# Kernel optimization log

Hardware: AMD Instinct MI355X
Metric: run time of the kernel (lower is better)

## Reference

```python
import jax, jax.numpy as jnp
import numpy as np

KQ_SIZE = 256  # kq_size from init


def setup_inputs() -> dict:
    key = jax.random.key(0)
    ks = jax.random.split(key, 8)
    B, N, V, KQ = 8, 4096, 1024, KQ_SIZE
    return {
        "input": jax.random.normal(ks[0], (B, N, V), dtype=jnp.float32),
        "Wq": jax.random.normal(ks[1], (V, KQ), dtype=jnp.float32) * 0.02,
        "bq": jax.random.normal(ks[2], (V,), dtype=jnp.float32) * 0.02,
        "Wk": jax.random.normal(ks[3], (V, KQ), dtype=jnp.float32) * 0.02,
        "bk": jax.random.normal(ks[4], (V,), dtype=jnp.float32) * 0.02,
        "Wv": jax.random.normal(ks[5], (V, V), dtype=jnp.float32) * 0.02,
        "bv": jax.random.normal(ks[6], (V,), dtype=jnp.float32) * 0.02,
        "gamma": jax.random.normal(ks[7], (1,), dtype=jnp.float32),
    }


def reference(input, Wq, bq, Wk, bk, Wv, bv, gamma):
    # input: [B, N, V]; flag=False -> kq slice is the LAST KQ_SIZE features
    kq = input[:, :, -KQ_SIZE:]                      # [B, N, KQ]
    q = jnp.einsum('bnk,vk->bnv', kq, Wq) + bq        # [B, N, V]
    k = jnp.einsum('bnk,vk->bnv', kq, Wk) + bk        # [B, N, V]
    v = jnp.einsum('bne,ve->bnv', input, Wv) + bv     # [B, N, V]
    # attn = bmm(k^T, q): feature-feature attention, NO 1/sqrt(d) scale
    attn = jnp.einsum('bnv,bnw->bvw', k, q)           # [B, V, V]
    attn = jax.nn.softmax(attn, axis=-1)
    out = jnp.einsum('bnv,bvw->bnw', v, attn)         # [B, N, V]
    return gamma * out + input
```

## Files before the change

### kernel.cpp

```cpp
#include <hip/hip_runtime.h>

#define B_ 8
#define N_ 4096
#define V_ 1024
#define KQ_ 256
#define KQOFF 768

typedef unsigned short u16;
typedef unsigned int u32;
typedef __attribute__((ext_vector_type(8))) __bf16 bf16x8;
typedef __attribute__((ext_vector_type(4))) float f32x4;

__device__ __forceinline__ u16 f2bf(float f) {
    union { float f; u32 u; } v; v.f = f;
    u32 r = v.u + 0x7fffu + ((v.u >> 16) & 1u);
    return (u16)(r >> 16);
}
__device__ __forceinline__ float bf2f(u16 h) {
    union { u32 u; float f; } v; v.u = ((u32)h) << 16; return v.f;
}
__device__ __forceinline__ void gl_lds16(const void* g, void* l) {
    __builtin_amdgcn_global_load_lds((const __attribute__((address_space(1))) u32*)g,
                                     (__attribute__((address_space(3))) u32*)l, 16, 0, 0);
}


__global__ void k_sum_s(const float* __restrict__ in, float* __restrict__ s) {
    const int b = blockIdx.x, chunk = blockIdx.y, k = threadIdx.x;
    const float* p = in + ((size_t)b * N_ + (size_t)chunk * 256) * V_ + KQOFF + k;
    float acc = 0.f;
    for (int r = 0; r < 256; ++r) acc += p[(size_t)r * V_];
    atomicAdd(&s[b * KQ_ + k], acc);
}

__global__ void k_syrk(const float* __restrict__ in, float* __restrict__ S) {
    const int bz = blockIdx.z;
    const int b = bz >> 3, nc = bz & 7;
    const int i0 = blockIdx.x * 64, j0 = blockIdx.y * 64;
    __shared__ float As[16][64], Bs[16][64];
    const int tid = threadIdx.x, tx = tid & 15, ty = tid >> 4;
    const int lrow = tid >> 4, lcol = (tid & 15) * 4;
    float acc[4][4] = {};
    const float* Xb = in + (size_t)b * N_ * V_ + KQOFF;
    const int nbeg = nc * 512, nend = nbeg + 512;
    for (int n0 = nbeg; n0 < nend; n0 += 16) {
        const float* base = Xb + (size_t)(n0 + lrow) * V_;
        const float4 a4 = *(const float4*)(base + i0 + lcol);
        const float4 b4 = *(const float4*)(base + j0 + lcol);
        *(float4*)&As[lrow][lcol] = a4;
        *(float4*)&Bs[lrow][lcol] = b4;
        __syncthreads();
#pragma unroll
        for (int kk = 0; kk < 16; ++kk) {
            float ra[4], rb[4];
#pragma unroll
            for (int a = 0; a < 4; ++a) ra[a] = As[kk][ty * 4 + a];
#pragma unroll
            for (int q = 0; q < 4; ++q) rb[q] = Bs[kk][tx * 4 + q];
#pragma unroll
            for (int a = 0; a < 4; ++a)
#pragma unroll
                for (int q = 0; q < 4; ++q) acc[a][q] += ra[a] * rb[q];
        }
        __syncthreads();
    }
#pragma unroll
    for (int a = 0; a < 4; ++a)
#pragma unroll
        for (int q = 0; q < 4; ++q)
            atomicAdd(&S[((size_t)b * KQ_ + i0 + ty * 4 + a) * KQ_ + j0 + tx * 4 + q],
                      acc[a][q]);
}

__global__ void k_uv(const float* __restrict__ Wq, const float* __restrict__ Wk,
                     const float* __restrict__ s, float* __restrict__ u,
                     float* __restrict__ t) {
    const int b = blockIdx.x;
    const int w = blockIdx.y * 256 + threadIdx.x;
    __shared__ float sl[256];
    sl[threadIdx.x] = s[b * KQ_ + threadIdx.x];
    __syncthreads();
    float au = 0.f, at = 0.f;
    const float* qr = Wq + (size_t)w * KQ_;
    const float* kr = Wk + (size_t)w * KQ_;
    for (int i = 0; i < KQ_; ++i) { au += qr[i] * sl[i]; at += kr[i] * sl[i]; }
    u[b * V_ + w] = au;
    t[b * V_ + w] = at;
}

__global__ void k_wkS(const float* __restrict__ Wk, const float* __restrict__ S,
                      float* __restrict__ T) {
    const int b = blockIdx.z;
    const int i0 = blockIdx.x * 64, j0 = blockIdx.y * 64;
    __shared__ float As[64][17];
    __shared__ float Bs[16][64];
    const int tid = threadIdx.x, tx = tid & 15, ty = tid >> 4;
    const int ar = tid >> 2, ac = (tid & 3) * 4;
    const int br = tid >> 4, bc = (tid & 15) * 4;
    float acc[4][4] = {};
    for (int k0 = 0; k0 < KQ_; k0 += 16) {
        const float4 a4 = *(const float4*)(Wk + (size_t)(i0 + ar) * KQ_ + k0 + ac);
        As[ar][ac + 0] = a4.x; As[ar][ac + 1] = a4.y;
        As[ar][ac + 2] = a4.z; As[ar][ac + 3] = a4.w;
        const float4 b4 = *(const float4*)(S + ((size_t)b * KQ_ + k0 + br) * KQ_ + j0 + bc);
        *(float4*)&Bs[br][bc] = b4;
        __syncthreads();
#pragma unroll
        for (int kk = 0; kk < 16; ++kk) {
            float ra[4], rb[4];
#pragma unroll
            for (int a = 0; a < 4; ++a) ra[a] = As[ty * 4 + a][kk];
#pragma unroll
            for (int q = 0; q < 4; ++q) rb[q] = Bs[kk][tx * 4 + q];
#pragma unroll
            for (int a = 0; a < 4; ++a)
#pragma unroll
                for (int q = 0; q < 4; ++q) acc[a][q] += ra[a] * rb[q];
        }
        __syncthreads();
    }
#pragma unroll
    for (int a = 0; a < 4; ++a) {
        float4 o; o.x = acc[a][0]; o.y = acc[a][1]; o.z = acc[a][2]; o.w = acc[a][3];
        *(float4*)(T + ((size_t)b * V_ + i0 + ty * 4 + a) * KQ_ + j0 + tx * 4) = o;
    }
}

__global__ void k_logits(const float* __restrict__ T, const float* __restrict__ Wq,
                         const float* __restrict__ bk, const float* __restrict__ bq,
                         const float* __restrict__ u, const float* __restrict__ t,
                         float* __restrict__ L) {
    const int b = blockIdx.z;
    const int i0 = blockIdx.x * 64, j0 = blockIdx.y * 64;
    __shared__ float As[64][17], Bs[64][17];
    const int tid = threadIdx.x, tx = tid & 15, ty = tid >> 4;
    const int r = tid >> 2, c = (tid & 3) * 4;
    float acc[4][4] = {};
    for (int k0 = 0; k0 < KQ_; k0 += 16) {
        const float4 a4 = *(const float4*)(T + ((size_t)b * V_ + i0 + r) * KQ_ + k0 + c);
        As[r][c + 0] = a4.x; As[r][c + 1] = a4.y; As[r][c + 2] = a4.z; As[r][c + 3] = a4.w;
        const float4 b4 = *(const float4*)(Wq + (size_t)(j0 + r) * KQ_ + k0 + c);
        Bs[r][c + 0] = b4.x; Bs[r][c + 1] = b4.y; Bs[r][c + 2] = b4.z; Bs[r][c + 3] = b4.w;
        __syncthreads();
#pragma unroll
        for (int kk = 0; kk < 16; ++kk) {
            float ra[4], rb[4];
#pragma unroll
            for (int a = 0; a < 4; ++a) ra[a] = As[ty * 4 + a][kk];
#pragma unroll
            for (int q = 0; q < 4; ++q) rb[q] = Bs[tx * 4 + q][kk];
#pragma unroll
            for (int a = 0; a < 4; ++a)
#pragma unroll
                for (int q = 0; q < 4; ++q) acc[a][q] += ra[a] * rb[q];
        }
        __syncthreads();
    }
#pragma unroll
    for (int a = 0; a < 4; ++a) {
        const int v = i0 + ty * 4 + a;
        const float bkv = bk[v];
        const float tv = t[b * V_ + v];
        float4 o;
        float* po = (float*)&o;
#pragma unroll
        for (int q = 0; q < 4; ++q) {
            const int w = j0 + tx * 4 + q;
            po[q] = acc[a][q] + bkv * (u[b * V_ + w] + 4096.0f * bq[w]) + tv * bq[w];
        }
        *(float4*)(L + ((size_t)b * V_ + v) * V_ + j0 + tx * 4) = o;
    }
}

__global__ void k_softmax(float* __restrict__ L) {
    const size_t row = blockIdx.x;
    float* p = L + row * V_;
    const int t = threadIdx.x;
    float vals[4];
    float m = -3.4e38f;
#pragma unroll
    for (int i = 0; i < 4; ++i) { vals[i] = p[t + i * 256]; m = fmaxf(m, vals[i]); }
    __shared__ float red[256];
    red[t] = m; __syncthreads();
    for (int s2 = 128; s2 > 0; s2 >>= 1) {
        if (t < s2) red[t] = fmaxf(red[t], red[t + s2]);
        __syncthreads();
    }
    m = red[0]; __syncthreads();
    float sum = 0.f;
#pragma unroll
    for (int i = 0; i < 4; ++i) { vals[i] = __expf(vals[i] - m); sum += vals[i]; }
    red[t] = sum; __syncthreads();
    for (int s2 = 128; s2 > 0; s2 >>= 1) {
        if (t < s2) red[t] += red[t + s2];
        __syncthreads();
    }
    const float inv = 1.f / red[0];
#pragma unroll
    for (int i = 0; i < 4; ++i) p[t + i * 256] = vals[i] * inv;
}

__global__ void k_transpose_cast(const float* __restrict__ src, u16* __restrict__ dst,
                                 size_t sbs, size_t dbs) {
    const float* s = src + (size_t)blockIdx.z * sbs;
    u16* d = dst + (size_t)blockIdx.z * dbs;
    __shared__ u16 tile[64][65];
    const int r0 = blockIdx.y * 64, c0 = blockIdx.x * 64;
    const int t = threadIdx.x;
#pragma unroll
    for (int rr = 0; rr < 16; ++rr) {
        const int row = rr * 4 + (t >> 6);
        tile[row][t & 63] = f2bf(s[(size_t)(r0 + row) * 1024 + c0 + (t & 63)]);
    }
    __syncthreads();
#pragma unroll
    for (int rr = 0; rr < 8; ++rr) {
        const int wrow = rr * 8 + (t >> 5);
        const int wc = (t & 31) * 2;
        ushort2 o; o.x = tile[wc][wrow]; o.y = tile[wc + 1][wrow];
        *(ushort2*)(d + (size_t)(c0 + wrow) * 1024 + r0 + wc) = o;
    }
}

__global__ void k_cvec(const u16* __restrict__ attnT, const float* __restrict__ bv,
                       float* __restrict__ c) {
    const int b = blockIdx.x;
    const int w = blockIdx.y * 4 + (threadIdx.x >> 6);
    const int lane = threadIdx.x & 63;
    const u16* row = attnT + ((size_t)b * V_ + w) * V_;
    float acc = 0.f;
#pragma unroll
    for (int ch = 0; ch < 2; ++ch) {
        const int v0 = ch * 512 + lane * 8;
        const uint4 pk = *(const uint4*)(row + v0);
        const u32 ws[4] = {pk.x, pk.y, pk.z, pk.w};
#pragma unroll
        for (int q = 0; q < 4; ++q) {
            acc += bf2f((u16)(ws[q] & 0xffffu)) * bv[v0 + 2 * q];
            acc += bf2f((u16)(ws[q] >> 16)) * bv[v0 + 2 * q + 1];
        }
    }
    for (int off = 32; off; off >>= 1) acc += __shfl_down(acc, off);
    if (lane == 0) c[b * V_ + w] = acc;
}

__global__ void k_C_mfma(const u16* __restrict__ At, const u16* __restrict__ Bt,
                         u16* __restrict__ Ct) {
    const int b = blockIdx.z;
    const int m0 = blockIdx.y * 128, n0 = blockIdx.x * 128;
    const u16* Ab = At + (size_t)b * V_ * V_;
    __shared__ u16 As[128 * 32], Bs[128 * 32];
    const int tid = threadIdx.x, lane = tid & 63, wave = tid >> 6;
    const int wm = wave & 1, wn = wave >> 1;
    const int srow = tid >> 2, scol = (tid & 3) * 8;
    f32x4 acc[4][4] = {};
    for (int k0 = 0; k0 < V_; k0 += 32) {
        gl_lds16(Ab + (size_t)(m0 + srow) * V_ + k0 + scol, As + tid * 8);
        gl_lds16(Ab + (size_t)(m0 + 64 + srow) * V_ + k0 + scol, As + (256 + tid) * 8);
        gl_lds16(Bt + (size_t)(n0 + srow) * V_ + k0 + scol, Bs + tid * 8);
        gl_lds16(Bt + (size_t)(n0 + 64 + srow) * V_ + k0 + scol, Bs + (256 + tid) * 8);
        __syncthreads();
        bf16x8 af[4], bfr[4];
#pragma unroll
        for (int i = 0; i < 4; ++i)
            af[i] = *(const bf16x8*)(As + (wm * 64 + i * 16 + (lane & 15)) * 32 + (lane >> 4) * 8);
#pragma unroll
        for (int j = 0; j < 4; ++j)
            bfr[j] = *(const bf16x8*)(Bs + (wn * 64 + j * 16 + (lane & 15)) * 32 + (lane >> 4) * 8);
#pragma unroll
        for (int i = 0; i < 4; ++i)
#pragma unroll
            for (int j = 0; j < 4; ++j)
                acc[i][j] = __builtin_amdgcn_mfma_f32_16x16x32_bf16(af[i], bfr[j], acc[i][j], 0, 0, 0);
        __syncthreads();
    }
    u16* Cb = Ct + (size_t)b * V_ * V_;
    const int quad = lane >> 4, col = lane & 15;
#pragma unroll
    for (int i = 0; i < 4; ++i)
#pragma unroll
        for (int j = 0; j < 4; ++j)
#pragma unroll
            for (int r = 0; r < 4; ++r)
                Cb[(size_t)(m0 + wm * 64 + i * 16 + quad * 4 + r) * V_ +
                   n0 + wn * 64 + j * 16 + col] = f2bf(acc[i][j][r]);
}

__global__ void k_out_mfma(const float* __restrict__ in, const u16* __restrict__ Ct,
                           const float* __restrict__ cvec, const float* __restrict__ gamma,
                           float* __restrict__ out) {
    const int id = blockIdx.x;
    const int agrp = ((id >> 6) << 3) | (id & 7);
    const int wtile = (id >> 3) & 7;
    const int b = agrp >> 5, ntile = agrp & 31;
    const int m0 = ntile * 128, n0 = wtile * 128;
    const float* Ain = in + (size_t)b * N_ * V_;
    const u16* Btb = Ct + (size_t)b * V_ * V_;
    __shared__ u16 As[128 * 32], Bs[128 * 32];
    const int tid = threadIdx.x, lane = tid & 63, wave = tid >> 6;
    const int wm = wave & 1, wn = wave >> 1;
    const int brow = tid >> 2, bcol = (tid & 3) * 8;
    const int arow = tid >> 3, acol = (tid & 7) * 4;
    f32x4 acc[4][4] = {};
    for (int k0 = 0; k0 < V_; k0 += 32) {
        gl_lds16(Btb + (size_t)(n0 + brow) * V_ + k0 + bcol, Bs + tid * 8);
        gl_lds16(Btb + (size_t)(n0 + 64 + brow) * V_ + k0 + bcol, Bs + (256 + tid) * 8);
#pragma unroll
        for (int ii = 0; ii < 4; ++ii) {
            const int row = arow + 32 * ii;
            const float4 v = *(const float4*)(Ain + (size_t)(m0 + row) * V_ + k0 + acol);
            const u32 ux = __builtin_bit_cast(u32, v.x) + 0x8000u;
            const u32 uy = __builtin_bit_cast(u32, v.y) + 0x8000u;
            const u32 uz = __builtin_bit_cast(u32, v.z) + 0x8000u;
            const u32 uw = __builtin_bit_cast(u32, v.w) + 0x8000u;
            uint2 p;
            p.x = __builtin_amdgcn_perm(uy, ux, 0x07060302u);
            p.y = __builtin_amdgcn_perm(uw, uz, 0x07060302u);
            *(uint2*)(As + row * 32 + acol) = p;
        }
        __syncthreads();
        bf16x8 af[4], bfr[4];
#pragma unroll
        for (int i = 0; i < 4; ++i)
            af[i] = *(const bf16x8*)(As + (wm * 64 + i * 16 + (lane & 15)) * 32 + (lane >> 4) * 8);
#pragma unroll
        for (int j = 0; j < 4; ++j)
            bfr[j] = *(const bf16x8*)(Bs + (wn * 64 + j * 16 + (lane & 15)) * 32 + (lane >> 4) * 8);
#pragma unroll
        for (int i = 0; i < 4; ++i)
#pragma unroll
            for (int j = 0; j < 4; ++j)
                acc[i][j] = __builtin_amdgcn_mfma_f32_16x16x32_bf16(af[i], bfr[j], acc[i][j], 0, 0, 0);
        __syncthreads();
    }
    const float g = gamma[0];
    const int quad = lane >> 4, col = lane & 15;
#pragma unroll
    for (int j = 0; j < 4; ++j) {
        const int n = n0 + wn * 64 + j * 16 + col;
        const float cv = cvec[b * V_ + n];
#pragma unroll
        for (int i = 0; i < 4; ++i) {
            const int mb = m0 + wm * 64 + i * 16 + quad * 4;
#pragma unroll
            for (int r = 0; r < 4; ++r) {
                const size_t off = (size_t)(b * N_ + mb + r) * V_ + n;
                out[off] = g * (acc[i][j][r] + cv) + in[off];
            }
        }
    }
}

extern "C" void kernel_launch(void* const* d_in, const int* in_sizes, int n_in,
                              void* d_out, int out_size, void* d_ws, size_t ws_size,
                              hipStream_t stream) {
    const float* in    = (const float*)d_in[0];
    const float* Wq    = (const float*)d_in[1];
    const float* bq    = (const float*)d_in[2];
    const float* Wk    = (const float*)d_in[3];
    const float* bk    = (const float*)d_in[4];
    const float* Wv    = (const float*)d_in[5];
    const float* bv    = (const float*)d_in[6];
    const float* gamma = (const float*)d_in[7];
    float* out = (float*)d_out;
    float* ws = (float*)d_ws;

    float* S   = ws + 0;
    u16*   WvT = (u16*)(ws + 0);
    float* sv  = ws + 524288;
    float* T   = ws + 526336;
    float* u   = ws + 2623488;
    float* tt  = ws + 2631680;
    float* L   = ws + 2639872;
    u16*   aT  = (u16*)(ws + 11028480);
    u16*   Ct  = (u16*)(ws + 15222784);
    float* cv  = ws + 19417088;

    hipMemsetAsync(S, 0, (size_t)(524288 + 2048) * sizeof(float), stream);

    k_sum_s  <<<dim3(8, 16),     256, 0, stream>>>(in, sv);
    k_syrk   <<<dim3(4, 4, 64),  256, 0, stream>>>(in, S);
    k_uv     <<<dim3(8, 4),      256, 0, stream>>>(Wq, Wk, sv, u, tt);
    k_wkS    <<<dim3(16, 4, 8),  256, 0, stream>>>(Wk, S, T);
    k_transpose_cast<<<dim3(16, 16, 1), 256, 0, stream>>>(Wv, WvT, 0, 0);
    k_logits <<<dim3(16, 16, 8), 256, 0, stream>>>(T, Wq, bk, bq, u, tt, L);
    k_softmax<<<8192,            256, 0, stream>>>(L);
    k_transpose_cast<<<dim3(16, 16, 8), 256, 0, stream>>>(L, aT, (size_t)V_ * V_, (size_t)V_ * V_);
    k_cvec   <<<dim3(8, 256),    256, 0, stream>>>(aT, bv, cv);
    k_C_mfma <<<dim3(8, 8, 8),   256, 0, stream>>>(aT, WvT, Ct);
    k_out_mfma<<<2048,           256, 0, stream>>>(in, Ct, cv, gamma, out);
}
```

Baseline: 668.0 us.

## Double-buffer B tiles and load A fragments directly from global in output GEMM

The output GEMM kernel now double-buffers the B (Ct) tile in LDS, prefetching the next k-slice while computing the current one, and drops one barrier per iteration. The A operand is no longer staged through LDS. Each wave reads its fp32 input fragments straight from global memory and packs them to bf16 in registers. The packing now truncates instead of rounding, and two waves load the same A rows redundantly, which doubles A global traffic through cache.

```diff
diff --git a/kernel.cpp b/kernel.cpp
--- a/kernel.cpp
+++ b/kernel.cpp
@@ -296,42 +296,47 @@
     const int m0 = ntile * 128, n0 = wtile * 128;
     const float* Ain = in + (size_t)b * N_ * V_;
     const u16* Btb = Ct + (size_t)b * V_ * V_;
-    __shared__ u16 As[128 * 32], Bs[128 * 32];
+    __shared__ u16 Bs[2][128 * 32];
     const int tid = threadIdx.x, lane = tid & 63, wave = tid >> 6;
     const int wm = wave & 1, wn = wave >> 1;
     const int brow = tid >> 2, bcol = (tid & 3) * 8;
-    const int arow = tid >> 3, acol = (tid & 7) * 4;
+    const float* Abase = Ain + (size_t)(m0 + wm * 64 + (lane & 15)) * V_ + (lane >> 4) * 8;
     f32x4 acc[4][4] = {};
-    for (int k0 = 0; k0 < V_; k0 += 32) {
-        gl_lds16(Btb + (size_t)(n0 + brow) * V_ + k0 + bcol, Bs + tid * 8);
-        gl_lds16(Btb + (size_t)(n0 + 64 + brow) * V_ + k0 + bcol, Bs + (256 + tid) * 8);
-#pragma unroll
-        for (int ii = 0; ii < 4; ++ii) {
-            const int row = arow + 32 * ii;
-            const float4 v = *(const float4*)(Ain + (size_t)(m0 + row) * V_ + k0 + acol);
-            const u32 ux = __builtin_bit_cast(u32, v.x) + 0x8000u;
-            const u32 uy = __builtin_bit_cast(u32, v.y) + 0x8000u;
-            const u32 uz = __builtin_bit_cast(u32, v.z) + 0x8000u;
-            const u32 uw = __builtin_bit_cast(u32, v.w) + 0x8000u;
-            uint2 p;
-            p.x = __builtin_amdgcn_perm(uy, ux, 0x07060302u);
-            p.y = __builtin_amdgcn_perm(uw, uz, 0x07060302u);
-            *(uint2*)(As + row * 32 + acol) = p;
-        }
-        __syncthreads();
-        bf16x8 af[4], bfr[4];
-#pragma unroll
-        for (int i = 0; i < 4; ++i)
-            af[i] = *(const bf16x8*)(As + (wm * 64 + i * 16 + (lane & 15)) * 32 + (lane >> 4) * 8);
+
+    gl_lds16(Btb + (size_t)(n0 + brow) * V_ + bcol, Bs[0] + tid * 8);
+    gl_lds16(Btb + (size_t)(n0 + 64 + brow) * V_ + bcol, Bs[0] + (256 + tid) * 8);
+
+    for (int it = 0; it < 32; ++it) {
+        const int cur = it & 1;
+        const int k0 = it * 32;
+        __syncthreads();
+        if (it + 1 < 32) {
+            const int kn = k0 + 32;
+            gl_lds16(Btb + (size_t)(n0 + brow) * V_ + kn + bcol, Bs[cur ^ 1] + tid * 8);
+            gl_lds16(Btb + (size_t)(n0 + 64 + brow) * V_ + kn + bcol, Bs[cur ^ 1] + (256 + tid) * 8);
+        }
+        bf16x8 af[4];
+#pragma unroll
+        for (int i = 0; i < 4; ++i) {
+            const float* p = Abase + (size_t)(i * 16) * V_ + k0;
+            const uint4 lo = *(const uint4*)(p);
+            const uint4 hi = *(const uint4*)(p + 4);
+            uint4 pk;
+            pk.x = __builtin_amdgcn_perm(lo.y, lo.x, 0x07060302u);
+            pk.y = __builtin_amdgcn_perm(lo.w, lo.z, 0x07060302u);
+            pk.z = __builtin_amdgcn_perm(hi.y, hi.x, 0x07060302u);
+            pk.w = __builtin_amdgcn_perm(hi.w, hi.z, 0x07060302u);
+            af[i] = __builtin_bit_cast(bf16x8, pk);
+        }
+        bf16x8 bfr[4];
 #pragma unroll
         for (int j = 0; j < 4; ++j)
-            bfr[j] = *(const bf16x8*)(Bs + (wn * 64 + j * 16 + (lane & 15)) * 32 + (lane >> 4) * 8);
+            bfr[j] = *(const bf16x8*)(Bs[cur] + (wn * 64 + j * 16 + (lane & 15)) * 32 + (lane >> 4) * 8);
 #pragma unroll
         for (int i = 0; i < 4; ++i)
 #pragma unroll
             for (int j = 0; j < 4; ++j)
                 acc[i][j] = __builtin_amdgcn_mfma_f32_16x16x32_bf16(af[i], bfr[j], acc[i][j], 0, 0, 0);
-        __syncthreads();
     }
     const float g = gamma[0];
     const int quad = lane >> 4, col = lane & 15;
```

Result: slower. 797.0 us (+19.3%).
